# Kernel optimization log

Hardware: AMD Instinct MI355X
Metric: run time of the kernel (lower is better)

## Reference

```python
import jax, jax.numpy as jnp
import numpy as np

NUM_NODES = 100000
NODE_DIM = 128
MEM_DIM = 128
EDGE_DIM = 172
TIME_DIM = 100
HIDDEN = 256
E = 262144


def setup_inputs() -> dict:
    key = jax.random.key(0)
    ks = jax.random.split(key, 12)
    src = jax.random.randint(ks[0], (E,), 0, NUM_NODES)
    dst = jax.random.randint(ks[1], (E,), 0, NUM_NODES)
    ts = jax.random.uniform(ks[2], (E,), dtype=jnp.float32) * 1e6
    edge_feat = jax.random.normal(ks[3], (E, EDGE_DIM), dtype=jnp.float32)
    node_emb = jax.random.normal(ks[4], (NUM_NODES, NODE_DIM), dtype=jnp.float32) * 0.02
    memory = jax.random.normal(ks[5], (NUM_NODES, MEM_DIM), dtype=jnp.float32) * 0.02
    # TimeEncoder: w.weight = 1/10**linspace(0,9,time_dim), bias = 0
    time_w = jnp.asarray(1.0 / 10 ** np.linspace(0, 9, TIME_DIM), dtype=jnp.float32)
    time_b = jnp.zeros((TIME_DIM,), dtype=jnp.float32)
    edge_W = jax.random.normal(ks[6], (HIDDEN, EDGE_DIM), dtype=jnp.float32) * (1.0 / np.sqrt(EDGE_DIM))
    edge_b = jnp.zeros((HIDDEN,), dtype=jnp.float32)
    in1 = NODE_DIM * 2 + MEM_DIM * 2  # 512
    W1 = jax.random.normal(ks[7], (HIDDEN, in1), dtype=jnp.float32) * (1.0 / np.sqrt(in1))
    b1 = jnp.zeros((HIDDEN,), dtype=jnp.float32)
    W2 = jax.random.normal(ks[8], (1, HIDDEN), dtype=jnp.float32) * (1.0 / np.sqrt(HIDDEN))
    b2 = jnp.zeros((1,), dtype=jnp.float32)
    return {
        "src": src, "dst": dst, "ts": ts, "edge_feat": edge_feat,
        "node_emb": node_emb, "memory": memory,
        "time_w": time_w, "time_b": time_b,
        "edge_W": edge_W, "edge_b": edge_b,
        "W1": W1, "b1": b1, "W2": W2, "b2": b2,
    }


def reference(src, dst, ts, edge_feat, node_emb, memory, time_w, time_b,
              edge_W, edge_b, W1, b1, W2, b2):
    # gathers (node embedding + memory table)
    src_embed = node_emb[src]          # [E, node_dim]
    dst_embed = node_emb[dst]          # [E, node_dim]
    src_memory = memory[src]           # [E, mem_dim]
    dst_memory = memory[dst]           # [E, mem_dim]
    # time / edge encodings are computed in the torch forward but unused in the output
    _time_embed = jnp.cos(ts[:, None] * time_w[None, :] + time_b)
    _edge_embed = edge_feat @ edge_W.T + edge_b
    # concat + 2-layer MLP scorer (Dropout is identity in eval)
    h = jnp.concatenate([src_embed, dst_embed, src_memory, dst_memory], axis=1)  # [E, 512]
    h1 = jax.nn.relu(h @ W1.T + b1)    # [E, hidden]
    out = (h1 @ W2.T + b2).squeeze(-1)  # [E]
    return out
```

## Files before the change

kernel.cpp:

```cpp
#include <hip/hip_runtime.h>

#define NNODES 100000
#define EDGES  262144
#define NTILES 3125
#define GEMM_BLOCKS 256

typedef __attribute__((ext_vector_type(8))) short short8v;
typedef __attribute__((ext_vector_type(8))) unsigned short ushort8v;
typedef __attribute__((ext_vector_type(4))) unsigned short ushort4v;
typedef __attribute__((ext_vector_type(4))) float f32x4;

__device__ __forceinline__ unsigned short f2bf(float f) {
  unsigned u = __builtin_bit_cast(unsigned, f);
  u += 0x7fffu + ((u >> 16) & 1u);
  return (unsigned short)(u >> 16);
}
__device__ __forceinline__ float bf2f(unsigned short u) {
  return __builtin_bit_cast(float, (unsigned)u << 16);
}

__global__ __launch_bounds__(256) void prep_wc(const float* __restrict__ W1,
                                               unsigned short* __restrict__ Wc) {
  int idx = blockIdx.x * 256 + threadIdx.x;
  int j = idx >> 8;
  int k = idx & 255;
  int jj = j & 255;
  int kk = (k < 128) ? k : (k + 128);
  if (j >= 256) kk += 128;
  Wc[idx] = f2bf(W1[jj * 512 + kk]);
}

__global__ __launch_bounds__(512, 2) void gemm_proj2(const float* __restrict__ ne,
                                                     const float* __restrict__ mem,
                                                     const unsigned short* __restrict__ Wc,
                                                     const float* __restrict__ b1,
                                                     unsigned short* __restrict__ P) {
  __shared__ __align__(16) unsigned short As[2][32][264];
  const int tid  = threadIdx.x;
  const int bid  = blockIdx.x;
  const int wid  = tid >> 6;
  const int lane = tid & 63;
  const int lr   = lane & 15;
  const int kq   = (lane >> 4) * 8;
  const int cb   = wid * 64;

  ushort8v bfrag[8][4];
#pragma unroll
  for (int ks = 0; ks < 8; ++ks)
#pragma unroll
    for (int ct = 0; ct < 4; ++ct)
      bfrag[ks][ct] = *(const ushort8v*)(Wc + (size_t)(cb + ct * 16 + lr) * 256 + ks * 32 + kq);

  float badd[4];
#pragma unroll
  for (int ct = 0; ct < 4; ++ct)
    badd[ct] = (cb < 256) ? b1[cb + ct * 16 + lr] : 0.0f;

  const int nt = (NTILES - bid + GEMM_BLOCKS - 1) / GEMM_BLOCKS;

  float4 g[4];
#pragma unroll
  for (int i = 0; i < 4; ++i) {
    int q = tid + i * 512;
    int row = q >> 6;
    int k0  = (q & 63) * 4;
    int node = bid * 32 + row;
    g[i] = *(const float4*)((k0 < 128) ? ne + (size_t)node * 128 + k0
                                       : mem + (size_t)node * 128 + (k0 - 128));
  }
#pragma unroll
  for (int i = 0; i < 4; ++i) {
    int q = tid + i * 512;
    int row = q >> 6;
    int k0  = (q & 63) * 4;
    ushort4v o;
    o[0] = f2bf(g[i].x); o[1] = f2bf(g[i].y); o[2] = f2bf(g[i].z); o[3] = f2bf(g[i].w);
    *(ushort4v*)&As[0][row][k0] = o;
  }
  __syncthreads();

  for (int it = 0; it < nt; ++it) {
    const int tile = bid + it * GEMM_BLOCKS;
    const int buf  = it & 1;

    const bool more = (it + 1 < nt);
    if (more) {
      const int ntile = bid + (it + 1) * GEMM_BLOCKS;
#pragma unroll
      for (int i = 0; i < 4; ++i) {
        int q = tid + i * 512;
        int row = q >> 6;
        int k0  = (q & 63) * 4;
        int node = ntile * 32 + row;
        g[i] = *(const float4*)((k0 < 128) ? ne + (size_t)node * 128 + k0
                                           : mem + (size_t)node * 128 + (k0 - 128));
      }
    }

    f32x4 acc[2][4] = {};
#pragma unroll
    for (int ks = 0; ks < 8; ++ks) {
      const int kk = ks * 32 + kq;
      ushort8v a0 = *(const ushort8v*)&As[buf][lr][kk];
      ushort8v a1 = *(const ushort8v*)&As[buf][lr + 16][kk];
#pragma unroll
      for (int ct = 0; ct < 4; ++ct) {
        acc[0][ct] = __builtin_amdgcn_mfma_f32_16x16x32_bf16((short8v)a0, (short8v)bfrag[ks][ct], acc[0][ct], 0, 0, 0);
        acc[1][ct] = __builtin_amdgcn_mfma_f32_16x16x32_bf16((short8v)a1, (short8v)bfrag[ks][ct], acc[1][ct], 0, 0, 0);
      }
    }

#pragma unroll
    for (int rt = 0; rt < 2; ++rt)
#pragma unroll
      for (int ct = 0; ct < 4; ++ct)
#pragma unroll
        for (int r = 0; r < 4; ++r) {
          int row  = rt * 16 + (lane >> 4) * 4 + r;
          int node = tile * 32 + row;
          P[(size_t)node * 512 + cb + ct * 16 + lr] = f2bf(acc[rt][ct][r] + badd[ct]);
        }

    if (more) {
#pragma unroll
      for (int i = 0; i < 4; ++i) {
        int q = tid + i * 512;
        int row = q >> 6;
        int k0  = (q & 63) * 4;
        ushort4v o;
        o[0] = f2bf(g[i].x); o[1] = f2bf(g[i].y); o[2] = f2bf(g[i].z); o[3] = f2bf(g[i].w);
        *(ushort4v*)&As[buf ^ 1][row][k0] = o;
      }
    }
    __syncthreads();
  }
}

__global__ __launch_bounds__(256) void edge_score(const int* __restrict__ src,
                                                  const int* __restrict__ dst,
                                                  const unsigned short* __restrict__ P,
                                                  const float* __restrict__ W2,
                                                  const float* __restrict__ b2,
                                                  float* __restrict__ out) {
  const int wid  = threadIdx.x >> 6;
  const int lane = threadIdx.x & 63;
  const int e    = blockIdx.x * 4 + wid;

  float4 w2v = *(const float4*)(W2 + lane * 4);
  const int s = src[e];
  const int d = dst[e];

  ushort4v a = *(const ushort4v*)(P + (size_t)s * 512 + lane * 4);
  ushort4v b = *(const ushort4v*)(P + (size_t)d * 512 + 256 + lane * 4);

  float h0 = bf2f(a[0]) + bf2f(b[0]); h0 = h0 > 0.f ? h0 : 0.f;
  float h1 = bf2f(a[1]) + bf2f(b[1]); h1 = h1 > 0.f ? h1 : 0.f;
  float h2 = bf2f(a[2]) + bf2f(b[2]); h2 = h2 > 0.f ? h2 : 0.f;
  float h3 = bf2f(a[3]) + bf2f(b[3]); h3 = h3 > 0.f ? h3 : 0.f;
  float partial = h0 * w2v.x + h1 * w2v.y + h2 * w2v.z + h3 * w2v.w;

#pragma unroll
  for (int off = 32; off; off >>= 1) partial += __shfl_xor(partial, off, 64);

  if (lane == 0) out[e] = partial + b2[0];
}

__global__ __launch_bounds__(256) void fallback_edge(const int* __restrict__ src,
                                                     const int* __restrict__ dst,
                                                     const float* __restrict__ ne,
                                                     const float* __restrict__ mem,
                                                     const float* __restrict__ W1,
                                                     const float* __restrict__ b1,
                                                     const float* __restrict__ W2,
                                                     const float* __restrict__ b2,
                                                     float* __restrict__ out) {
  __shared__ float hs[8][512];
  __shared__ float red[8][4];
  const int tid = threadIdx.x;
  const int e0  = blockIdx.x * 8;

  for (int idx = tid; idx < 8 * 512; idx += 256) {
    int e8 = idx >> 9, k = idx & 511;
    int e = e0 + e8;
    int s = src[e], d = dst[e];
    float v;
    if (k < 128)      v = ne[(size_t)s * 128 + k];
    else if (k < 256) v = ne[(size_t)d * 128 + k - 128];
    else if (k < 384) v = mem[(size_t)s * 128 + k - 256];
    else              v = mem[(size_t)d * 128 + k - 384];
    hs[e8][k] = v;
  }
  __syncthreads();

  const int j = tid;
  float acc[8] = {0, 0, 0, 0, 0, 0, 0, 0};
  const float* w1r = W1 + (size_t)j * 512;
  for (int k = 0; k < 512; k += 4) {
    float4 w = *(const float4*)(w1r + k);
#pragma unroll
    for (int e8 = 0; e8 < 8; ++e8)
      acc[e8] += hs[e8][k] * w.x + hs[e8][k + 1] * w.y + hs[e8][k + 2] * w.z + hs[e8][k + 3] * w.w;
  }
  const float bj = b1[j], wj = W2[j];
#pragma unroll
  for (int e8 = 0; e8 < 8; ++e8) {
    float h = acc[e8] + bj;
    h = h > 0.f ? h : 0.f;
    acc[e8] = h * wj;
  }
  const int lane = tid & 63, wid = tid >> 6;
#pragma unroll
  for (int e8 = 0; e8 < 8; ++e8) {
    float p = acc[e8];
#pragma unroll
    for (int off = 32; off; off >>= 1) p += __shfl_xor(p, off, 64);
    if (lane == 0) red[e8][wid] = p;
  }
  __syncthreads();
  if (tid < 8) out[e0 + tid] = red[tid][0] + red[tid][1] + red[tid][2] + red[tid][3] + b2[0];
}

extern "C" void kernel_launch(void* const* d_in, const int* in_sizes, int n_in,
                              void* d_out, int out_size, void* d_ws, size_t ws_size,
                              hipStream_t stream) {
  const int*   src      = (const int*)d_in[0];
  const int*   dst      = (const int*)d_in[1];
  const float* node_emb = (const float*)d_in[4];
  const float* memv     = (const float*)d_in[5];
  const float* W1       = (const float*)d_in[10];
  const float* b1       = (const float*)d_in[11];
  const float* W2       = (const float*)d_in[12];
  const float* b2       = (const float*)d_in[13];
  float*       out      = (float*)d_out;

  const size_t P_BYTES  = (size_t)NNODES * 512 * 2;
  const size_t WC_BYTES = (size_t)512 * 256 * 2;

  if (ws_size >= P_BYTES + WC_BYTES) {
    unsigned short* P  = (unsigned short*)d_ws;
    unsigned short* Wc = (unsigned short*)((char*)d_ws + P_BYTES);
    prep_wc<<<512, 256, 0, stream>>>(W1, Wc);
    gemm_proj2<<<GEMM_BLOCKS, 512, 0, stream>>>(node_emb, memv, Wc, b1, P);
    edge_score<<<EDGES / 4, 256, 0, stream>>>(src, dst, P, W2, b2, out);
  } else {
    fallback_edge<<<EDGES / 8, 256, 0, stream>>>(src, dst, node_emb, memv, W1, b1, W2, b2, out);
  }
}
```

Before: 101.6 us.

## Fuse W1 bf16 conversion into GEMM, transpose MFMA output, widen edge gathers

Removes the separate prep_wc kernel launch: each GEMM wave now loads W1 in fp32 and converts it into its bf16 B fragments inline. The MFMA operands are swapped so each lane holds four contiguous output columns, which lets the P writeback use packed 8-byte stores via v_cvt_pk_bf16_f32 instead of scattered 2-byte stores. The edge scoring kernel now handles two edges per wave with 16-byte gathers and a shorter shuffle reduction. The cost is redundant W1 loading and conversion in every block, plus use of inline asm for the packed conversion.

```diff
diff --git a/kernel.cpp b/kernel.cpp
--- a/kernel.cpp
+++ b/kernel.cpp
@@ -18,21 +18,15 @@
 __device__ __forceinline__ float bf2f(unsigned short u) {
   return __builtin_bit_cast(float, (unsigned)u << 16);
 }
-
-__global__ __launch_bounds__(256) void prep_wc(const float* __restrict__ W1,
-                                               unsigned short* __restrict__ Wc) {
-  int idx = blockIdx.x * 256 + threadIdx.x;
-  int j = idx >> 8;
-  int k = idx & 255;
-  int jj = j & 255;
-  int kk = (k < 128) ? k : (k + 128);
-  if (j >= 256) kk += 128;
-  Wc[idx] = f2bf(W1[jj * 512 + kk]);
-}
-
-__global__ __launch_bounds__(512, 2) void gemm_proj2(const float* __restrict__ ne,
+__device__ __forceinline__ unsigned cvt_pk(float lo, float hi) {
+  unsigned r;
+  asm volatile("v_cvt_pk_bf16_f32 %0, %1, %2" : "=v"(r) : "v"(lo), "v"(hi));
+  return r;
+}
+
+__global__ __launch_bounds__(512, 2) void gemm_proj3(const float* __restrict__ ne,
                                                      const float* __restrict__ mem,
-                                                     const unsigned short* __restrict__ Wc,
+                                                     const float* __restrict__ W1,
                                                      const float* __restrict__ b1,
                                                      unsigned short* __restrict__ P) {
   __shared__ __align__(16) unsigned short As[2][32][264];
@@ -46,15 +40,27 @@
 
   ushort8v bfrag[8][4];
 #pragma unroll
-  for (int ks = 0; ks < 8; ++ks)
-#pragma unroll
-    for (int ct = 0; ct < 4; ++ct)
-      bfrag[ks][ct] = *(const ushort8v*)(Wc + (size_t)(cb + ct * 16 + lr) * 256 + ks * 32 + kq);
-
-  float badd[4];
-#pragma unroll
-  for (int ct = 0; ct < 4; ++ct)
-    badd[ct] = (cb < 256) ? b1[cb + ct * 16 + lr] : 0.0f;
+  for (int ks = 0; ks < 8; ++ks) {
+#pragma unroll
+    for (int jt = 0; jt < 4; ++jt) {
+      int j  = cb + jt * 16 + lr;
+      int jj = j & 255;
+      int kk = ks * 32 + kq + (ks >= 4 ? 128 : 0) + (j >= 256 ? 128 : 0);
+      float4 wlo = *(const float4*)(W1 + (size_t)jj * 512 + kk);
+      float4 whi = *(const float4*)(W1 + (size_t)jj * 512 + kk + 4);
+      ushort8v f;
+      f[0] = f2bf(wlo.x); f[1] = f2bf(wlo.y); f[2] = f2bf(wlo.z); f[3] = f2bf(wlo.w);
+      f[4] = f2bf(whi.x); f[5] = f2bf(whi.y); f[6] = f2bf(whi.z); f[7] = f2bf(whi.w);
+      bfrag[ks][jt] = f;
+    }
+  }
+
+  float4 b1v[4];
+#pragma unroll
+  for (int jt = 0; jt < 4; ++jt) {
+    if (cb < 256) b1v[jt] = *(const float4*)(b1 + cb + jt * 16 + (lane >> 4) * 4);
+    else          b1v[jt] = float4{0.f, 0.f, 0.f, 0.f};
+  }
 
   const int nt = (NTILES - bid + GEMM_BLOCKS - 1) / GEMM_BLOCKS;
 
@@ -73,17 +79,16 @@
     int q = tid + i * 512;
     int row = q >> 6;
     int k0  = (q & 63) * 4;
-    ushort4v o;
-    o[0] = f2bf(g[i].x); o[1] = f2bf(g[i].y); o[2] = f2bf(g[i].z); o[3] = f2bf(g[i].w);
-    *(ushort4v*)&As[0][row][k0] = o;
+    uint2 pk { cvt_pk(g[i].x, g[i].y), cvt_pk(g[i].z, g[i].w) };
+    *(uint2*)&As[0][row][k0] = pk;
   }
   __syncthreads();
 
   for (int it = 0; it < nt; ++it) {
     const int tile = bid + it * GEMM_BLOCKS;
     const int buf  = it & 1;
-
     const bool more = (it + 1 < nt);
+
     if (more) {
       const int ntile = bid + (it + 1) * GEMM_BLOCKS;
 #pragma unroll
@@ -97,29 +102,29 @@
       }
     }
 
-    f32x4 acc[2][4] = {};
+    f32x4 acc[4][2] = {};
 #pragma unroll
     for (int ks = 0; ks < 8; ++ks) {
       const int kk = ks * 32 + kq;
       ushort8v a0 = *(const ushort8v*)&As[buf][lr][kk];
       ushort8v a1 = *(const ushort8v*)&As[buf][lr + 16][kk];
 #pragma unroll
-      for (int ct = 0; ct < 4; ++ct) {
-        acc[0][ct] = __builtin_amdgcn_mfma_f32_16x16x32_bf16((short8v)a0, (short8v)bfrag[ks][ct], acc[0][ct], 0, 0, 0);
-        acc[1][ct] = __builtin_amdgcn_mfma_f32_16x16x32_bf16((short8v)a1, (short8v)bfrag[ks][ct], acc[1][ct], 0, 0, 0);
-      }
-    }
-
-#pragma unroll
-    for (int rt = 0; rt < 2; ++rt)
-#pragma unroll
-      for (int ct = 0; ct < 4; ++ct)
-#pragma unroll
-        for (int r = 0; r < 4; ++r) {
-          int row  = rt * 16 + (lane >> 4) * 4 + r;
-          int node = tile * 32 + row;
-          P[(size_t)node * 512 + cb + ct * 16 + lr] = f2bf(acc[rt][ct][r] + badd[ct]);
-        }
+      for (int jt = 0; jt < 4; ++jt) {
+        acc[jt][0] = __builtin_amdgcn_mfma_f32_16x16x32_bf16((short8v)bfrag[ks][jt], (short8v)a0, acc[jt][0], 0, 0, 0);
+        acc[jt][1] = __builtin_amdgcn_mfma_f32_16x16x32_bf16((short8v)bfrag[ks][jt], (short8v)a1, acc[jt][1], 0, 0, 0);
+      }
+    }
+
+#pragma unroll
+    for (int jt = 0; jt < 4; ++jt)
+#pragma unroll
+      for (int h = 0; h < 2; ++h) {
+        int node = tile * 32 + h * 16 + lr;
+        f32x4 v = acc[jt][h];
+        uint2 pk { cvt_pk(v[0] + b1v[jt].x, v[1] + b1v[jt].y),
+                   cvt_pk(v[2] + b1v[jt].z, v[3] + b1v[jt].w) };
+        *(uint2*)(P + (size_t)node * 512 + cb + jt * 16 + (lane >> 4) * 4) = pk;
+      }
 
     if (more) {
 #pragma unroll
@@ -127,42 +132,52 @@
         int q = tid + i * 512;
         int row = q >> 6;
         int k0  = (q & 63) * 4;
-        ushort4v o;
-        o[0] = f2bf(g[i].x); o[1] = f2bf(g[i].y); o[2] = f2bf(g[i].z); o[3] = f2bf(g[i].w);
-        *(ushort4v*)&As[buf ^ 1][row][k0] = o;
+        uint2 pk { cvt_pk(g[i].x, g[i].y), cvt_pk(g[i].z, g[i].w) };
+        *(uint2*)&As[buf ^ 1][row][k0] = pk;
       }
     }
     __syncthreads();
   }
 }
 
-__global__ __launch_bounds__(256) void edge_score(const int* __restrict__ src,
-                                                  const int* __restrict__ dst,
-                                                  const unsigned short* __restrict__ P,
-                                                  const float* __restrict__ W2,
-                                                  const float* __restrict__ b2,
-                                                  float* __restrict__ out) {
+__global__ __launch_bounds__(256) void edge_score2(const int* __restrict__ src,
+                                                   const int* __restrict__ dst,
+                                                   const unsigned short* __restrict__ P,
+                                                   const float* __restrict__ W2,
+                                                   const float* __restrict__ b2,
+                                                   float* __restrict__ out) {
   const int wid  = threadIdx.x >> 6;
   const int lane = threadIdx.x & 63;
-  const int e    = blockIdx.x * 4 + wid;
-
-  float4 w2v = *(const float4*)(W2 + lane * 4);
+  const int half = lane >> 5;
+  const int l5   = lane & 31;
+  const int e    = blockIdx.x * 8 + wid * 2 + half;
+
+  float4 w0 = *(const float4*)(W2 + l5 * 8);
+  float4 w1 = *(const float4*)(W2 + l5 * 8 + 4);
+  const float b2c = b2[0];
+
   const int s = src[e];
   const int d = dst[e];
 
-  ushort4v a = *(const ushort4v*)(P + (size_t)s * 512 + lane * 4);
-  ushort4v b = *(const ushort4v*)(P + (size_t)d * 512 + 256 + lane * 4);
+  ushort8v a = *(const ushort8v*)(P + (size_t)s * 512 + l5 * 8);
+  ushort8v b = *(const ushort8v*)(P + (size_t)d * 512 + 256 + l5 * 8);
 
   float h0 = bf2f(a[0]) + bf2f(b[0]); h0 = h0 > 0.f ? h0 : 0.f;
   float h1 = bf2f(a[1]) + bf2f(b[1]); h1 = h1 > 0.f ? h1 : 0.f;
   float h2 = bf2f(a[2]) + bf2f(b[2]); h2 = h2 > 0.f ? h2 : 0.f;
   float h3 = bf2f(a[3]) + bf2f(b[3]); h3 = h3 > 0.f ? h3 : 0.f;
-  float partial = h0 * w2v.x + h1 * w2v.y + h2 * w2v.z + h3 * w2v.w;
-
-#pragma unroll
-  for (int off = 32; off; off >>= 1) partial += __shfl_xor(partial, off, 64);
-
-  if (lane == 0) out[e] = partial + b2[0];
+  float h4 = bf2f(a[4]) + bf2f(b[4]); h4 = h4 > 0.f ? h4 : 0.f;
+  float h5 = bf2f(a[5]) + bf2f(b[5]); h5 = h5 > 0.f ? h5 : 0.f;
+  float h6 = bf2f(a[6]) + bf2f(b[6]); h6 = h6 > 0.f ? h6 : 0.f;
+  float h7 = bf2f(a[7]) + bf2f(b[7]); h7 = h7 > 0.f ? h7 : 0.f;
+
+  float partial = h0 * w0.x + h1 * w0.y + h2 * w0.z + h3 * w0.w
+                + h4 * w1.x + h5 * w1.y + h6 * w1.z + h7 * w1.w;
+
+#pragma unroll
+  for (int off = 16; off; off >>= 1) partial += __shfl_xor(partial, off, 64);
+
+  if (l5 == 0) out[e] = partial + b2c;
 }
 
 __global__ __launch_bounds__(256) void fallback_edge(const int* __restrict__ src,
@@ -233,15 +248,12 @@
   const float* b2       = (const float*)d_in[13];
   float*       out      = (float*)d_out;
 
-  const size_t P_BYTES  = (size_t)NNODES * 512 * 2;
-  const size_t WC_BYTES = (size_t)512 * 256 * 2;
-
-  if (ws_size >= P_BYTES + WC_BYTES) {
-    unsigned short* P  = (unsigned short*)d_ws;
-    unsigned short* Wc = (unsigned short*)((char*)d_ws + P_BYTES);
-    prep_wc<<<512, 256, 0, stream>>>(W1, Wc);
-    gemm_proj2<<<GEMM_BLOCKS, 512, 0, stream>>>(node_emb, memv, Wc, b1, P);
-    edge_score<<<EDGES / 4, 256, 0, stream>>>(src, dst, P, W2, b2, out);
+  const size_t P_BYTES = (size_t)NNODES * 512 * 2;
+
+  if (ws_size >= P_BYTES) {
+    unsigned short* P = (unsigned short*)d_ws;
+    gemm_proj3<<<GEMM_BLOCKS, 512, 0, stream>>>(node_emb, memv, W1, b1, P);
+    edge_score2<<<EDGES / 8, 256, 0, stream>>>(src, dst, P, W2, b2, out);
   } else {
     fallback_edge<<<EDGES / 8, 256, 0, stream>>>(src, dst, node_emb, memv, W1, b1, W2, b2, out);
   }
```

Result: slower. 130.4 us (+28.3%).
